# Optimization experiments

Hardware: AMD Instinct MI355X
Metric: run time of the kernel (lower is better)

Reference implementation:

```python
import jax, jax.numpy as jnp
import numpy as np

N_SOC = 100_000   # nodes in social_neighbour_g (== embedding rows)
N_I2U = 50_000    # nodes in item2user_g
E_SOC = 1_600_000
E_I2U = 800_000
F = 128           # embedding_size (num_heads = 1)


def gatv2(src, dst, num_nodes, feat, Ws, bs, Wd, bd, attn):
    """DGL GATv2Conv, num_heads=1, share_weights=False, activation=leaky_relu."""
    el = feat @ Ws + bs                     # [N, F] fc_src
    er = feat @ Wd + bd                     # [N, F] fc_dst
    e = jax.nn.leaky_relu(el[src] + er[dst], 0.2)   # [E, F]
    s = e @ attn                            # [E] attention logits
    # edge softmax grouped by destination node
    m = jax.ops.segment_max(s, dst, num_segments=num_nodes)
    ex = jnp.exp(s - m[dst])
    den = jax.ops.segment_sum(ex, dst, num_segments=num_nodes)
    alpha = ex / den[dst]                   # [E]
    out = jax.ops.segment_sum(el[src] * alpha[:, None], dst, num_segments=num_nodes)
    return jax.nn.leaky_relu(out, 0.01)     # module-level activation (default slope)


def setup_inputs() -> dict:
    key = jax.random.key(0)
    ks = jax.random.split(key, 16)
    sc = 1.0 / np.sqrt(F)
    inp = {
        "embedding": jax.random.normal(ks[0], (N_SOC, F), jnp.float32),
        "i2u_src": jax.random.randint(ks[1], (E_I2U,), 0, N_I2U, jnp.int32),
        "i2u_dst": jax.random.randint(ks[2], (E_I2U,), 0, N_I2U, jnp.int32),
        "i2u_nid": jnp.arange(N_I2U, dtype=jnp.int32),  # unique global IDs of subgraph nodes
        "soc_src": jax.random.randint(ks[3], (E_SOC,), 0, N_SOC, jnp.int32),
        "soc_dst": jax.random.randint(ks[4], (E_SOC,), 0, N_SOC, jnp.int32),
        "Wsrc1": jax.random.normal(ks[5], (F, F), jnp.float32) * sc,
        "bsrc1": jnp.zeros((F,), jnp.float32),
        "Wdst1": jax.random.normal(ks[6], (F, F), jnp.float32) * sc,
        "bdst1": jnp.zeros((F,), jnp.float32),
        "attn1": jax.random.normal(ks[7], (F,), jnp.float32) * sc,
        "Wsrc2": jax.random.normal(ks[8], (F, F), jnp.float32) * sc,
        "bsrc2": jnp.zeros((F,), jnp.float32),
        "Wdst2": jax.random.normal(ks[9], (F, F), jnp.float32) * sc,
        "bdst2": jnp.zeros((F,), jnp.float32),
        "attn2": jax.random.normal(ks[10], (F,), jnp.float32) * sc,
    }
    return inp


def reference(embedding, i2u_src, i2u_dst, i2u_nid, soc_src, soc_dst,
              Wsrc1, bsrc1, Wdst1, bdst1, attn1,
              Wsrc2, bsrc2, Wdst2, bdst2, attn2):
    # social_used_embedding = embedding[item2user_g.ndata['_ID']]
    used = embedding[i2u_nid]                                   # [N_i2u, F]
    h1 = gatv2(i2u_src, i2u_dst, i2u_nid.shape[0], used,
               Wsrc1, bsrc1, Wdst1, bdst1, attn1)               # [N_i2u, F]
    # social_embedding = embedding[social_g.nodes()]  (nodes() == arange(N_soc))
    soc = embedding
    # used_user_id = where(sum(h1, dim=1) != 0); scatter those rows via _ID
    mask = jnp.sum(h1, axis=1) != 0                              # [N_i2u]
    upd = jnp.where(mask[:, None], h1, soc[i2u_nid])
    soc = soc.at[i2u_nid].set(upd)
    out = gatv2(soc_src, soc_dst, soc.shape[0], soc,
                Wsrc2, bsrc2, Wdst2, bdst2, attn2)               # [N_soc, F]
    return out
```

## Files before the change

kernel.cpp:

```cpp
#include <hip/hip_runtime.h>
#include <hip/hip_fp16.h>
#include <math.h>

#define F 128
#define BSHIFT 9
#define BSIZE  512
#define BMAX   200
#define CHUNK  4096
#define PKSTR  12288

#define APAD 8
#define ASTR (F + APAD)

typedef _Float16 half8_t __attribute__((ext_vector_type(8)));
typedef _Float16 half4_t __attribute__((ext_vector_type(4)));
typedef float f32x4 __attribute__((ext_vector_type(4)));

#define PK_ADD(d, a, b) asm("v_pk_add_f16 %0, %1, %2" : "=v"(d) : "v"(a), "v"(b))
#define PK_MUL(d, a, b) asm("v_pk_mul_f16 %0, %1, %2" : "=v"(d) : "v"(a), "v"(b))
#define PK_MAX(d, a, b) asm("v_pk_max_f16 %0, %1, %2" : "=v"(d) : "v"(a), "v"(b))
#define FMA_MIX_LO(acc, h2u, f) \
    asm("v_fma_mix_f32 %0, %1, %2, %0 op_sel_hi:[1,0,0]" : "+v"(acc) : "v"(h2u), "v"(f))
#define FMA_MIX_HI(acc, h2u, f) \
    asm("v_fma_mix_f32 %0, %1, %2, %0 op_sel:[1,0,0] op_sel_hi:[1,0,0]" : "+v"(acc) : "v"(h2u), "v"(f))

__device__ __forceinline__ float row_sum16(float x) {
    int y;
    y = __builtin_amdgcn_update_dpp(0, __float_as_int(x), 0x121, 0xf, 0xf, true);
    x += __int_as_float(y);
    y = __builtin_amdgcn_update_dpp(0, __float_as_int(x), 0x122, 0xf, 0xf, true);
    x += __int_as_float(y);
    y = __builtin_amdgcn_update_dpp(0, __float_as_int(x), 0x124, 0xf, 0xf, true);
    x += __int_as_float(y);
    y = __builtin_amdgcn_update_dpp(0, __float_as_int(x), 0x128, 0xf, 0xf, true);
    x += __int_as_float(y);
    return x;
}

__global__ __launch_bounds__(256) void k_scatter(
        const int* __restrict__ src1, const int* __restrict__ dst1, int E1,
        int* __restrict__ bcur1, unsigned* __restrict__ pk1, int C1,
        const int* __restrict__ src2, const int* __restrict__ dst2, int E2,
        int* __restrict__ bcur2, unsigned* __restrict__ pk2, int C2,
        const int* __restrict__ nid, int Nn, int* __restrict__ inv, int CI,
        const float* __restrict__ Ws1, const float* __restrict__ Wd1,
        const float* __restrict__ bs1, const float* __restrict__ bd1,
        const float* __restrict__ at1,
        __half* __restrict__ wt1, float* __restrict__ bp1, float* __restrict__ ap1,
        const float* __restrict__ Ws2, const float* __restrict__ Wd2,
        const float* __restrict__ bs2, const float* __restrict__ bd2,
        const float* __restrict__ at2,
        __half* __restrict__ wt2, float* __restrict__ bp2, float* __restrict__ ap2) {
    int b = blockIdx.x, t = threadIdx.x;
    __shared__ int hist[BMAX];
    __shared__ int cur[BMAX];
    if (b < C1 + C2) {
        const int* src; const int* dst; int E; int* bcur; unsigned* pk; int c;
        if (b < C1) { src = src1; dst = dst1; E = E1; bcur = bcur1; pk = pk1; c = b; }
        else        { src = src2; dst = dst2; E = E2; bcur = bcur2; pk = pk2; c = b - C1; }
        for (int i = t; i < BMAX; i += 256) hist[i] = 0;
        __syncthreads();
        int e0 = c * CHUNK;
        int dc[CHUNK / 256], sc[CHUNK / 256];
#pragma unroll
        for (int i = 0; i < CHUNK / 256; i++) {
            int e = e0 + t + i * 256;
            if (e < E) {
                int d = dst[e];
                dc[i] = d; sc[i] = src[e];
                atomicAdd(&hist[d >> BSHIFT], 1);
            } else {
                dc[i] = -1;
            }
        }
        __syncthreads();
        for (int i = t; i < BMAX; i += 256) {
            int n = hist[i];
            if (n) cur[i] = atomicAdd(&bcur[i], n);
        }
        __syncthreads();
#pragma unroll
        for (int i = 0; i < CHUNK / 256; i++) {
            int d = dc[i];
            if (d >= 0) {
                int bb = d >> BSHIFT;
                int pos = atomicAdd(&cur[bb], 1);
                if (pos < PKSTR)
                    pk[(size_t)bb * PKSTR + pos] =
                        ((unsigned)(d & (BSIZE - 1)) << 17) | (unsigned)sc[i];
            }
        }
    } else if (b < C1 + C2 + CI) {
        int i0 = (b - C1 - C2) * CHUNK + t;
#pragma unroll
        for (int k = 0; k < CHUNK / 256; k++) {
            int j = i0 + k * 256;
            if (j < Nn) inv[nid[j]] = j;
        }
    } else {
        int wb = b - (C1 + C2 + CI);
        int layer = wb >> 3, bl = wb & 7;
        const float* Ws = layer ? Ws2 : Ws1;
        const float* Wd = layer ? Wd2 : Wd1;
        __half* wt = layer ? wt2 : wt1;
#pragma unroll
        for (int i = 0; i < 16; i++) {
            int e = bl * 4096 + i * 256 + t;
            int n = e >> 7, k = e & 127;
            float v = (n < 128) ? Ws[k * 128 + n] : Wd[k * 128 + (n - 128)];
            wt[(size_t)n * 128 + k] = __float2half(v);
        }
        if (bl == 0) {
            const float* bs = layer ? bs2 : bs1;
            const float* bd = layer ? bd2 : bd1;
            const float* at = layer ? at2 : at1;
            float* bp = layer ? bp2 : bp1;
            float* ap = layer ? ap2 : ap1;
            bp[t] = (t < 128) ? bs[t] : bd[t - 128];
            if (t < 128) ap[t] = at[t] * 1.44269504f;
        }
    }
}

__device__ __forceinline__ void finesort_body(unsigned* __restrict__ pk,
        const int* __restrict__ bcur, int b, int N,
        int* __restrict__ rpb, int* __restrict__ rpe) {
    __shared__ int cnt[BSIZE];
    __shared__ int cur[BSIZE];
    __shared__ int tps[256];
    int t = threadIdx.x;
    int node0 = b << BSHIFT;
    int base = b * PKSTR;
    int ne = bcur[b]; if (ne > PKSTR) ne = PKSTR;
    unsigned* pkb = pk + (size_t)base;
    cnt[t] = 0; cnt[t + 256] = 0;
    __syncthreads();
    unsigned stash[PKSTR / 256];
#pragma unroll
    for (int k = 0; k < PKSTR / 256; k++) {
        int i = t + k * 256;
        unsigned v = 0xFFFFFFFFu;
        if (i < ne) { v = pkb[i]; atomicAdd(&cnt[v >> 17], 1); }
        stash[k] = v;
    }
    __syncthreads();
    int s0 = cnt[2 * t], s1 = cnt[2 * t + 1];
    int tp = s0 + s1;
    tps[t] = tp;
    __syncthreads();
    for (int off = 1; off < 256; off <<= 1) {
        int x = (t >= off) ? tps[t - off] : 0;
        __syncthreads();
        tps[t] += x;
        __syncthreads();
    }
    int excl = tps[t] - tp;
    int c0 = base + excl, c1 = c0 + s0;
    cur[2 * t] = c0; cur[2 * t + 1] = c1;
    int n0 = node0 + 2 * t, n1 = n0 + 1;
    if (n0 < N) { rpb[n0] = c0; rpe[n0] = c0 + s0; }
    if (n1 < N) { rpb[n1] = c1; rpe[n1] = c1 + s1; }
    __syncthreads();
    int* outb = (int*)pk;
#pragma unroll
    for (int k = 0; k < PKSTR / 256; k++) {
        unsigned v = stash[k];
        if (v != 0xFFFFFFFFu) {
            int dl = v >> 17;
            int pos = atomicAdd(&cur[dl], 1);
            outb[pos] = (int)(v & 0x1FFFFu);
        }
    }
}

__device__ __forceinline__ void gemm_mfma_body(int blk,
        const float* __restrict__ emb, const int* __restrict__ nid,
        const float* __restrict__ h1, const int* __restrict__ inv, const int* __restrict__ flag,
        int Nrows,
        const __half* __restrict__ wt, const float* __restrict__ bp,
        __half* __restrict__ el, __half* __restrict__ er) {
    __shared__ _Float16 As[64 * ASTR];
    __shared__ const float* rps[64];
    int t = threadIdx.x;
    int row0 = blk * 64;

    if (t < 64) {
        int grow = row0 + t;
        const float* rowp = nullptr;
        if (grow < Nrows) {
            if (inv) {
                int j = inv[grow];
                rowp = (j >= 0 && flag[j]) ? h1 + (size_t)j * F : emb + (size_t)grow * F;
            } else {
                int asrc = nid ? nid[grow] : grow;
                rowp = emb + (size_t)asrc * F;
            }
        }
        rps[t] = rowp;
    }
    __syncthreads();

#pragma unroll
    for (int i = 0; i < 8; i++) {
        int e = i * 256 + t;
        int r = e >> 5;
        int c = (e & 31) * 4;
        const float* rowp = rps[r];
        float4 v = make_float4(0.f, 0.f, 0.f, 0.f);
        if (rowp) v = *(const float4*)(rowp + c);
        half4_t hv = { (_Float16)v.x, (_Float16)v.y, (_Float16)v.z, (_Float16)v.w };
        *(half4_t*)(As + r * ASTR + c) = hv;
    }
    __syncthreads();

    int lane = t & 63, wave = t >> 6;
    int li = lane & 15, quad = lane >> 4;

    f32x4 acc[4][4];
#pragma unroll
    for (int a = 0; a < 4; a++)
#pragma unroll
        for (int b = 0; b < 4; b++) acc[a][b] = (f32x4){0.f, 0.f, 0.f, 0.f};

    const _Float16* wtp = (const _Float16*)wt;
#pragma unroll
    for (int ks = 0; ks < 4; ks++) {
        half8_t af[4], bf[4];
#pragma unroll
        for (int nt = 0; nt < 4; nt++)
            af[nt] = *(const half8_t*)(As + (nt * 16 + li) * ASTR + ks * 32 + quad * 8);
#pragma unroll
        for (int ft = 0; ft < 4; ft++) {
            int n = wave * 64 + ft * 16 + li;
            bf[ft] = *(const half8_t*)(wtp + (size_t)n * F + ks * 32 + quad * 8);
        }
#pragma unroll
        for (int ft = 0; ft < 4; ft++)
#pragma unroll
            for (int nt = 0; nt < 4; nt++)
                acc[ft][nt] = __builtin_amdgcn_mfma_f32_16x16x32_f16(
                    bf[ft], af[nt], acc[ft][nt], 0, 0, 0);
    }

    __half* dst = (wave < 2) ? el : er;
    int fb = (wave & 1) * 64 + quad * 4;
    f32x4 bv4[4];
#pragma unroll
    for (int ft = 0; ft < 4; ft++)
        bv4[ft] = *(const f32x4*)(bp + wave * 64 + ft * 16 + quad * 4);
#pragma unroll
    for (int nt = 0; nt < 4; nt++) {
        int node = row0 + nt * 16 + li;
        if (node < Nrows) {
#pragma unroll
            for (int ft = 0; ft < 4; ft++) {
                half4_t h4 = { (_Float16)(acc[ft][nt][0] + bv4[ft][0]),
                               (_Float16)(acc[ft][nt][1] + bv4[ft][1]),
                               (_Float16)(acc[ft][nt][2] + bv4[ft][2]),
                               (_Float16)(acc[ft][nt][3] + bv4[ft][3]) };
                *(half4_t*)(dst + (size_t)node * F + fb + ft * 16) = h4;
            }
        }
    }
}

__global__ __launch_bounds__(256, 4) void k_sortg1(
        unsigned* __restrict__ pk1, const int* __restrict__ bcur1, int B1, int N1,
        int* __restrict__ rpb1, int* __restrict__ rpe1,
        unsigned* __restrict__ pk2, const int* __restrict__ bcur2, int B2, int N2,
        int* __restrict__ rpb2, int* __restrict__ rpe2,
        const float* __restrict__ emb, const int* __restrict__ nid, int G1rows,
        const __half* __restrict__ wt1, const float* __restrict__ bp1,
        __half* __restrict__ el1, __half* __restrict__ er1) {
    int blk = blockIdx.x;
    if (blk < B1 + B2) {
        unsigned* pk; const int* bcur; int b, N; int* rpb; int* rpe;
        if (blk < B1) { pk = pk1; bcur = bcur1; b = blk;      N = N1; rpb = rpb1; rpe = rpe1; }
        else          { pk = pk2; bcur = bcur2; b = blk - B1; N = N2; rpb = rpb2; rpe = rpe2; }
        finesort_body(pk, bcur, b, N, rpb, rpe);
    } else {
        gemm_mfma_body(blk - (B1 + B2), emb, nid, nullptr, nullptr, nullptr,
                       G1rows, wt1, bp1, el1, er1);
    }
}

__global__ __launch_bounds__(256, 4) void gemm2_k(
        const float* __restrict__ emb, const float* __restrict__ h1,
        const int* __restrict__ inv, const int* __restrict__ flag, int Nrows,
        const __half* __restrict__ wt, const float* __restrict__ bp,
        __half* __restrict__ el, __half* __restrict__ er) {
    gemm_mfma_body(blockIdx.x, emb, nullptr, h1, inv, flag, Nrows, wt, bp, el, er);
}

__device__ __forceinline__ void agg_core(
        const int* __restrict__ rpb, const int* __restrict__ rpe,
        const int* __restrict__ srcs,
        const __half* __restrict__ el, const __half* __restrict__ er,
        const float* __restrict__ ap, int node, int g, int li,
        float* o, int& beg, int& end) {
    uint4 ru = *(const uint4*)(er + (size_t)node * F + li * 8);
    float av[8];
    *(float4*)(av + 0) = *(const float4*)(ap + li * 8 + 0);
    *(float4*)(av + 4) = *(const float4*)(ap + li * 8 + 4);

    beg = rpb[node]; end = rpe[node];
    float l = 0.f;
    float acc[8];
#pragma unroll
    for (int j = 0; j < 8; j++) acc[j] = 0.f;

    const unsigned C02 = 0x32663266u;

    auto dot_edge = [&](const uint4& V) -> float {
        float p = 0.f;
        unsigned x, y;
        PK_ADD(x, V.x, ru.x); PK_MUL(y, x, C02); PK_MAX(x, x, y);
        FMA_MIX_LO(p, x, av[0]); FMA_MIX_HI(p, x, av[1]);
        PK_ADD(x, V.y, ru.y); PK_MUL(y, x, C02); PK_MAX(x, x, y);
        FMA_MIX_LO(p, x, av[2]); FMA_MIX_HI(p, x, av[3]);
        PK_ADD(x, V.z, ru.z); PK_MUL(y, x, C02); PK_MAX(x, x, y);
        FMA_MIX_LO(p, x, av[4]); FMA_MIX_HI(p, x, av[5]);
        PK_ADD(x, V.w, ru.w); PK_MUL(y, x, C02); PK_MAX(x, x, y);
        FMA_MIX_LO(p, x, av[6]); FMA_MIX_HI(p, x, av[7]);
        return p;
    };
    auto acc_edge = [&](const uint4& V, float ex) {
        FMA_MIX_LO(acc[0], V.x, ex); FMA_MIX_HI(acc[1], V.x, ex);
        FMA_MIX_LO(acc[2], V.y, ex); FMA_MIX_HI(acc[3], V.y, ex);
        FMA_MIX_LO(acc[4], V.z, ex); FMA_MIX_HI(acc[5], V.z, ex);
        FMA_MIX_LO(acc[6], V.w, ex); FMA_MIX_HI(acc[7], V.w, ex);
    };
    auto compute4 = [&](const uint4& A, const uint4& B, const uint4& Cv, const uint4& D,
                        int cb0) {
        int c0 = cb0 + g * 4;
        bool v0 = c0 < end, v1 = c0 + 1 < end, v2 = c0 + 2 < end, v3 = c0 + 3 < end;
        float p0 = dot_edge(A), p1 = dot_edge(B), p2 = dot_edge(Cv), p3 = dot_edge(D);
        p0 = row_sum16(p0); p1 = row_sum16(p1);
        p2 = row_sum16(p2); p3 = row_sum16(p3);
        float x0 = v0 ? __builtin_amdgcn_exp2f(p0) : 0.f;
        float x1 = v1 ? __builtin_amdgcn_exp2f(p1) : 0.f;
        float x2 = v2 ? __builtin_amdgcn_exp2f(p2) : 0.f;
        float x3 = v3 ? __builtin_amdgcn_exp2f(p3) : 0.f;
        l += (x0 + x1) + (x2 + x3);
        acc_edge(A, x0); acc_edge(B, x1); acc_edge(Cv, x2); acc_edge(D, x3);
    };

    const __half* ep = el + li * 8;
    if (beg < end) {
        int e1 = end - 1;
        int I0, I1, I2, I3, J0, J1, J2, J3;
        {
            int a = beg + g * 4;
            I0 = __builtin_nontemporal_load(srcs + (a     < e1 ? a     : e1));
            I1 = __builtin_nontemporal_load(srcs + (a + 1 < e1 ? a + 1 : e1));
            I2 = __builtin_nontemporal_load(srcs + (a + 2 < e1 ? a + 2 : e1));
            I3 = __builtin_nontemporal_load(srcs + (a + 3 < e1 ? a + 3 : e1));
        }
        uint4 R0 = *(const uint4*)(ep + (size_t)I0 * F);
        uint4 R1 = *(const uint4*)(ep + (size_t)I1 * F);
        uint4 R2 = *(const uint4*)(ep + (size_t)I2 * F);
        uint4 R3 = *(const uint4*)(ep + (size_t)I3 * F);
        {
            int a = beg + 8 + g * 4;
            J0 = __builtin_nontemporal_load(srcs + (a     < e1 ? a     : e1));
            J1 = __builtin_nontemporal_load(srcs + (a + 1 < e1 ? a + 1 : e1));
            J2 = __builtin_nontemporal_load(srcs + (a + 2 < e1 ? a + 2 : e1));
            J3 = __builtin_nontemporal_load(srcs + (a + 3 < e1 ? a + 3 : e1));
        }
        int cb = beg;
        for (;;) {
            uint4 S0, S1, S2, S3;
            bool hn = (cb + 8) < end;
            if (hn) {
                S0 = *(const uint4*)(ep + (size_t)J0 * F);
                S1 = *(const uint4*)(ep + (size_t)J1 * F);
                S2 = *(const uint4*)(ep + (size_t)J2 * F);
                S3 = *(const uint4*)(ep + (size_t)J3 * F);
                int a = cb + 16 + g * 4;
                I0 = __builtin_nontemporal_load(srcs + (a     < e1 ? a     : e1));
                I1 = __builtin_nontemporal_load(srcs + (a + 1 < e1 ? a + 1 : e1));
                I2 = __builtin_nontemporal_load(srcs + (a + 2 < e1 ? a + 2 : e1));
                I3 = __builtin_nontemporal_load(srcs + (a + 3 < e1 ? a + 3 : e1));
            }
            compute4(R0, R1, R2, R3, cb);
            cb += 8;
            if (!hn) break;
            bool hn2 = (cb + 8) < end;
            if (hn2) {
                R0 = *(const uint4*)(ep + (size_t)I0 * F);
                R1 = *(const uint4*)(ep + (size_t)I1 * F);
                R2 = *(const uint4*)(ep + (size_t)I2 * F);
                R3 = *(const uint4*)(ep + (size_t)I3 * F);
                int a = cb + 16 + g * 4;
                J0 = __builtin_nontemporal_load(srcs + (a     < e1 ? a     : e1));
                J1 = __builtin_nontemporal_load(srcs + (a + 1 < e1 ? a + 1 : e1));
                J2 = __builtin_nontemporal_load(srcs + (a + 2 < e1 ? a + 2 : e1));
                J3 = __builtin_nontemporal_load(srcs + (a + 3 < e1 ? a + 3 : e1));
            }
            compute4(S0, S1, S2, S3, cb);
            cb += 8;
            if (!hn2) break;
        }
    }

    l += __shfl_xor(l, 16, 64);
#pragma unroll
    for (int j = 0; j < 8; j++) acc[j] += __shfl_xor(acc[j], 16, 64);

    if (end > beg) {
        float inv = 1.f / l;
#pragma unroll
        for (int j = 0; j < 8; j++) {
            float v = acc[j] * inv;
            o[j] = fmaxf(v, 0.01f * v);
        }
    } else {
#pragma unroll
        for (int j = 0; j < 8; j++) o[j] = 0.f;
    }
}

__global__ __launch_bounds__(256) void agg1_k(
        const int* __restrict__ rpb, const int* __restrict__ rpe,
        const int* __restrict__ srcs,
        const __half* __restrict__ el, const __half* __restrict__ er,
        const float* __restrict__ ap, int N,
        float* __restrict__ h1, int* __restrict__ flag) {
    int node = blockIdx.x * 8 + (threadIdx.x >> 5);
    if (node >= N) return;
    int t = threadIdx.x;
    int g = (t >> 4) & 1, li = t & 15;
    float o[8]; int beg, end;
    agg_core(rpb, rpe, srcs, el, er, ap, node, g, li, o, beg, end);

    float tot = 0.f;
#pragma unroll
    for (int j = 0; j < 8; j++) tot += o[j];
    tot = row_sum16(tot);
    if (g == 0) {
        *(float4*)(h1 + (size_t)node * F + li * 8 + 0) = *(float4*)(o + 0);
        *(float4*)(h1 + (size_t)node * F + li * 8 + 4) = *(float4*)(o + 4);
        if (li == 0) flag[node] = (tot != 0.f) ? 1 : 0;
    }
}

__global__ __launch_bounds__(256) void agg2_k(
        const int* __restrict__ rpb, const int* __restrict__ rpe,
        const int* __restrict__ srcs,
        const __half* __restrict__ el, const __half* __restrict__ er,
        const float* __restrict__ ap, int N, float* __restrict__ out) {
    int node = blockIdx.x * 8 + (threadIdx.x >> 5);
    if (node >= N) return;
    int t = threadIdx.x;
    int g = (t >> 4) & 1, li = t & 15;
    float o[8]; int beg, end;
    agg_core(rpb, rpe, srcs, el, er, ap, node, g, li, o, beg, end);
    if (g == 0) {
        *(float4*)(out + (size_t)node * F + li * 8 + 0) = *(float4*)(o + 0);
        *(float4*)(out + (size_t)node * F + li * 8 + 4) = *(float4*)(o + 4);
    }
}

static inline int cdiv(int a, int b) { return (a + b - 1) / b; }

extern "C" void kernel_launch(void* const* d_in, const int* in_sizes, int n_in,
                              void* d_out, int out_size, void* d_ws, size_t ws_size,
                              hipStream_t stream) {
    const float* emb   = (const float*)d_in[0];
    const int* i2u_src = (const int*)d_in[1];
    const int* i2u_dst = (const int*)d_in[2];
    const int* i2u_nid = (const int*)d_in[3];
    const int* soc_src = (const int*)d_in[4];
    const int* soc_dst = (const int*)d_in[5];
    const float* Ws1 = (const float*)d_in[6];
    const float* bs1 = (const float*)d_in[7];
    const float* Wd1 = (const float*)d_in[8];
    const float* bd1 = (const float*)d_in[9];
    const float* at1 = (const float*)d_in[10];
    const float* Ws2 = (const float*)d_in[11];
    const float* bs2 = (const float*)d_in[12];
    const float* Wd2 = (const float*)d_in[13];
    const float* bd2 = (const float*)d_in[14];
    const float* at2 = (const float*)d_in[15];

    const int N_soc = in_sizes[0] / F;
    const int E_i2u = in_sizes[1];
    const int N_i2u = in_sizes[3];
    const int E_soc = in_sizes[4];

    const int B1 = cdiv(N_i2u, BSIZE);
    const int B2 = cdiv(N_soc, BSIZE);
    const int C1 = cdiv(E_i2u, CHUNK);
    const int C2 = cdiv(E_soc, CHUNK);
    const int CI = cdiv(N_i2u, CHUNK);
    const int G1 = cdiv(N_i2u, 64);

    char* p = (char*)d_ws;
    auto carve = [&](size_t bytes) -> char* {
        char* r = p; p += (bytes + 255) & ~(size_t)255; return r;
    };
    __half* el1  = (__half*)carve((size_t)N_i2u * F * 2);
    __half* er1  = (__half*)carve((size_t)N_i2u * F * 2);
    __half* el2  = (__half*)carve((size_t)N_soc * F * 2);
    __half* er2  = (__half*)carve((size_t)N_soc * F * 2);
    float* h1buf = (float*)carve((size_t)N_i2u * F * 4);
    int* flag    = (int*)carve((size_t)N_i2u * 4);
    int* inv     = (int*)carve((size_t)N_soc * 4);

    unsigned* pk1 = (unsigned*)carve((size_t)B1 * PKSTR * 4);
    unsigned* pk2 = (unsigned*)carve((size_t)B2 * PKSTR * 4);
    int* rpb1    = (int*)carve((size_t)N_i2u * 4);
    int* rpe1    = (int*)carve((size_t)N_i2u * 4);
    int* rpb2    = (int*)carve((size_t)N_soc * 4);
    int* rpe2    = (int*)carve((size_t)N_soc * 4);

    int* bcur    = (int*)carve((size_t)(B1 + B2) * 4);
    int* bcur1 = bcur, *bcur2 = bcur + B1;

    __half* wt1  = (__half*)carve((size_t)256 * 128 * 2);
    __half* wt2  = (__half*)carve((size_t)256 * 128 * 2);
    float* bp1   = (float*)carve(256 * 4);
    float* bp2   = (float*)carve(256 * 4);
    float* ap1   = (float*)carve(128 * 4);
    float* ap2   = (float*)carve(128 * 4);

    (void)hipMemsetAsync(bcur, 0, (size_t)(B1 + B2) * 4, stream);
    (void)hipMemsetAsync(inv, 0xFF, (size_t)N_soc * 4, stream);

    k_scatter<<<C1 + C2 + CI + 16, 256, 0, stream>>>(
        i2u_src, i2u_dst, E_i2u, bcur1, pk1, C1,
        soc_src, soc_dst, E_soc, bcur2, pk2, C2,
        i2u_nid, N_i2u, inv, CI,
        Ws1, Wd1, bs1, bd1, at1, wt1, bp1, ap1,
        Ws2, Wd2, bs2, bd2, at2, wt2, bp2, ap2);

    k_sortg1<<<B1 + B2 + G1, 256, 0, stream>>>(
        pk1, bcur1, B1, N_i2u, rpb1, rpe1,
        pk2, bcur2, B2, N_soc, rpb2, rpe2,
        emb, i2u_nid, N_i2u, wt1, bp1, el1, er1);

    agg1_k<<<cdiv(N_i2u, 8), 256, 0, stream>>>(
        rpb1, rpe1, (const int*)pk1, el1, er1, ap1, N_i2u, h1buf, flag);

    gemm2_k<<<cdiv(N_soc, 64), 256, 0, stream>>>(emb, h1buf, inv, flag, N_soc, wt2, bp2, el2, er2);

    agg2_k<<<cdiv(N_soc, 8), 256, 0, stream>>>(
        rpb2, rpe2, (const int*)pk2, el2, er2, ap2, N_soc, (float*)d_out);
}
```

Baseline: 344.9 us.

## Use one 16-lane group per node in aggregation, drop dual-group split

The aggregation kernels change from two 16-lane groups per destination node (each taking alternate 4-edge chunks, then combined by cross-lane shuffles) to a single 16-lane group per node, packing 16 nodes per block. The deep double-buffered prefetch of gathered rows is replaced by a simple loop that only prefetches the next four source indices. The aim is to remove idle half-groups on low-degree nodes and the final shuffle reduction. In exchange each node's edges are processed serially with less memory-level parallelism, since gathered rows are no longer prefetched ahead.

```diff
diff --git a/kernel.cpp b/kernel.cpp
--- a/kernel.cpp
+++ b/kernel.cpp
@@ -296,7 +296,7 @@
         const int* __restrict__ rpb, const int* __restrict__ rpe,
         const int* __restrict__ srcs,
         const __half* __restrict__ el, const __half* __restrict__ er,
-        const float* __restrict__ ap, int node, int g, int li,
+        const float* __restrict__ ap, int node, int li,
         float* o, int& beg, int& end) {
     uint4 ru = *(const uint4*)(er + (size_t)node * F + li * 8);
     float av[8];
@@ -330,82 +330,40 @@
         FMA_MIX_LO(acc[4], V.z, ex); FMA_MIX_HI(acc[5], V.z, ex);
         FMA_MIX_LO(acc[6], V.w, ex); FMA_MIX_HI(acc[7], V.w, ex);
     };
-    auto compute4 = [&](const uint4& A, const uint4& B, const uint4& Cv, const uint4& D,
-                        int cb0) {
-        int c0 = cb0 + g * 4;
-        bool v0 = c0 < end, v1 = c0 + 1 < end, v2 = c0 + 2 < end, v3 = c0 + 3 < end;
-        float p0 = dot_edge(A), p1 = dot_edge(B), p2 = dot_edge(Cv), p3 = dot_edge(D);
-        p0 = row_sum16(p0); p1 = row_sum16(p1);
-        p2 = row_sum16(p2); p3 = row_sum16(p3);
-        float x0 = v0 ? __builtin_amdgcn_exp2f(p0) : 0.f;
-        float x1 = v1 ? __builtin_amdgcn_exp2f(p1) : 0.f;
-        float x2 = v2 ? __builtin_amdgcn_exp2f(p2) : 0.f;
-        float x3 = v3 ? __builtin_amdgcn_exp2f(p3) : 0.f;
-        l += (x0 + x1) + (x2 + x3);
-        acc_edge(A, x0); acc_edge(B, x1); acc_edge(Cv, x2); acc_edge(D, x3);
-    };
 
     const __half* ep = el + li * 8;
     if (beg < end) {
         int e1 = end - 1;
-        int I0, I1, I2, I3, J0, J1, J2, J3;
-        {
-            int a = beg + g * 4;
-            I0 = __builtin_nontemporal_load(srcs + (a     < e1 ? a     : e1));
-            I1 = __builtin_nontemporal_load(srcs + (a + 1 < e1 ? a + 1 : e1));
-            I2 = __builtin_nontemporal_load(srcs + (a + 2 < e1 ? a + 2 : e1));
-            I3 = __builtin_nontemporal_load(srcs + (a + 3 < e1 ? a + 3 : e1));
-        }
-        uint4 R0 = *(const uint4*)(ep + (size_t)I0 * F);
-        uint4 R1 = *(const uint4*)(ep + (size_t)I1 * F);
-        uint4 R2 = *(const uint4*)(ep + (size_t)I2 * F);
-        uint4 R3 = *(const uint4*)(ep + (size_t)I3 * F);
-        {
-            int a = beg + 8 + g * 4;
-            J0 = __builtin_nontemporal_load(srcs + (a     < e1 ? a     : e1));
-            J1 = __builtin_nontemporal_load(srcs + (a + 1 < e1 ? a + 1 : e1));
-            J2 = __builtin_nontemporal_load(srcs + (a + 2 < e1 ? a + 2 : e1));
-            J3 = __builtin_nontemporal_load(srcs + (a + 3 < e1 ? a + 3 : e1));
-        }
-        int cb = beg;
-        for (;;) {
-            uint4 S0, S1, S2, S3;
-            bool hn = (cb + 8) < end;
-            if (hn) {
-                S0 = *(const uint4*)(ep + (size_t)J0 * F);
-                S1 = *(const uint4*)(ep + (size_t)J1 * F);
-                S2 = *(const uint4*)(ep + (size_t)J2 * F);
-                S3 = *(const uint4*)(ep + (size_t)J3 * F);
-                int a = cb + 16 + g * 4;
-                I0 = __builtin_nontemporal_load(srcs + (a     < e1 ? a     : e1));
-                I1 = __builtin_nontemporal_load(srcs + (a + 1 < e1 ? a + 1 : e1));
-                I2 = __builtin_nontemporal_load(srcs + (a + 2 < e1 ? a + 2 : e1));
-                I3 = __builtin_nontemporal_load(srcs + (a + 3 < e1 ? a + 3 : e1));
+        int s0 = __builtin_nontemporal_load(srcs + beg);
+        int s1 = __builtin_nontemporal_load(srcs + (beg + 1 < e1 ? beg + 1 : e1));
+        int s2 = __builtin_nontemporal_load(srcs + (beg + 2 < e1 ? beg + 2 : e1));
+        int s3 = __builtin_nontemporal_load(srcs + (beg + 3 < e1 ? beg + 3 : e1));
+        for (int cb = beg; cb < end; cb += 4) {
+            bool v0 = cb < end, v1 = cb + 1 < end, v2 = cb + 2 < end, v3 = cb + 3 < end;
+            int t0 = s0, t1 = s1, t2 = s2, t3 = s3;
+            int nb = cb + 4;
+            if (nb < end) {
+                s0 = __builtin_nontemporal_load(srcs + (nb     < e1 ? nb     : e1));
+                s1 = __builtin_nontemporal_load(srcs + (nb + 1 < e1 ? nb + 1 : e1));
+                s2 = __builtin_nontemporal_load(srcs + (nb + 2 < e1 ? nb + 2 : e1));
+                s3 = __builtin_nontemporal_load(srcs + (nb + 3 < e1 ? nb + 3 : e1));
             }
-            compute4(R0, R1, R2, R3, cb);
-            cb += 8;
-            if (!hn) break;
-            bool hn2 = (cb + 8) < end;
-            if (hn2) {
-                R0 = *(const uint4*)(ep + (size_t)I0 * F);
-                R1 = *(const uint4*)(ep + (size_t)I1 * F);
-                R2 = *(const uint4*)(ep + (size_t)I2 * F);
-                R3 = *(const uint4*)(ep + (size_t)I3 * F);
-                int a = cb + 16 + g * 4;
-                J0 = __builtin_nontemporal_load(srcs + (a     < e1 ? a     : e1));
-                J1 = __builtin_nontemporal_load(srcs + (a + 1 < e1 ? a + 1 : e1));
-                J2 = __builtin_nontemporal_load(srcs + (a + 2 < e1 ? a + 2 : e1));
-                J3 = __builtin_nontemporal_load(srcs + (a + 3 < e1 ? a + 3 : e1));
-            }
-            compute4(S0, S1, S2, S3, cb);
-            cb += 8;
-            if (!hn2) break;
-        }
-    }
-
-    l += __shfl_xor(l, 16, 64);
-#pragma unroll
-    for (int j = 0; j < 8; j++) acc[j] += __shfl_xor(acc[j], 16, 64);
+            uint4 A  = *(const uint4*)(ep + (size_t)t0 * F);
+            uint4 B  = *(const uint4*)(ep + (size_t)t1 * F);
+            uint4 Cv = *(const uint4*)(ep + (size_t)t2 * F);
+            uint4 D  = *(const uint4*)(ep + (size_t)t3 * F);
+
+            float p0 = dot_edge(A), p1 = dot_edge(B), p2 = dot_edge(Cv), p3 = dot_edge(D);
+            p0 = row_sum16(p0); p1 = row_sum16(p1);
+            p2 = row_sum16(p2); p3 = row_sum16(p3);
+            float x0 = v0 ? __builtin_amdgcn_exp2f(p0) : 0.f;
+            float x1 = v1 ? __builtin_amdgcn_exp2f(p1) : 0.f;
+            float x2 = v2 ? __builtin_amdgcn_exp2f(p2) : 0.f;
+            float x3 = v3 ? __builtin_amdgcn_exp2f(p3) : 0.f;
+            l += (x0 + x1) + (x2 + x3);
+            acc_edge(A, x0); acc_edge(B, x1); acc_edge(Cv, x2); acc_edge(D, x3);
+        }
+    }
 
     if (end > beg) {
         float inv = 1.f / l;
@@ -426,22 +384,19 @@
         const __half* __restrict__ el, const __half* __restrict__ er,
         const float* __restrict__ ap, int N,
         float* __restrict__ h1, int* __restrict__ flag) {
-    int node = blockIdx.x * 8 + (threadIdx.x >> 5);
+    int node = blockIdx.x * 16 + (threadIdx.x >> 4);
     if (node >= N) return;
-    int t = threadIdx.x;
-    int g = (t >> 4) & 1, li = t & 15;
+    int li = threadIdx.x & 15;
     float o[8]; int beg, end;
-    agg_core(rpb, rpe, srcs, el, er, ap, node, g, li, o, beg, end);
+    agg_core(rpb, rpe, srcs, el, er, ap, node, li, o, beg, end);
 
     float tot = 0.f;
 #pragma unroll
     for (int j = 0; j < 8; j++) tot += o[j];
     tot = row_sum16(tot);
-    if (g == 0) {
-        *(float4*)(h1 + (size_t)node * F + li * 8 + 0) = *(float4*)(o + 0);
-        *(float4*)(h1 + (size_t)node * F + li * 8 + 4) = *(float4*)(o + 4);
-        if (li == 0) flag[node] = (tot != 0.f) ? 1 : 0;
-    }
+    *(float4*)(h1 + (size_t)node * F + li * 8 + 0) = *(float4*)(o + 0);
+    *(float4*)(h1 + (size_t)node * F + li * 8 + 4) = *(float4*)(o + 4);
+    if (li == 0) flag[node] = (tot != 0.f) ? 1 : 0;
 }
 
 __global__ __launch_bounds__(256) void agg2_k(
@@ -449,16 +404,13 @@
         const int* __restrict__ srcs,
         const __half* __restrict__ el, const __half* __restrict__ er,
         const float* __restrict__ ap, int N, float* __restrict__ out) {
-    int node = blockIdx.x * 8 + (threadIdx.x >> 5);
+    int node = blockIdx.x * 16 + (threadIdx.x >> 4);
     if (node >= N) return;
-    int t = threadIdx.x;
-    int g = (t >> 4) & 1, li = t & 15;
+    int li = threadIdx.x & 15;
     float o[8]; int beg, end;
-    agg_core(rpb, rpe, srcs, el, er, ap, node, g, li, o, beg, end);
-    if (g == 0) {
-        *(float4*)(out + (size_t)node * F + li * 8 + 0) = *(float4*)(o + 0);
-        *(float4*)(out + (size_t)node * F + li * 8 + 4) = *(float4*)(o + 4);
-    }
+    agg_core(rpb, rpe, srcs, el, er, ap, node, li, o, beg, end);
+    *(float4*)(out + (size_t)node * F + li * 8 + 0) = *(float4*)(o + 0);
+    *(float4*)(out + (size_t)node * F + li * 8 + 4) = *(float4*)(o + 4);
 }
 
 static inline int cdiv(int a, int b) { return (a + b - 1) / b; }
@@ -539,11 +491,11 @@
         pk2, bcur2, B2, N_soc, rpb2, rpe2,
         emb, i2u_nid, N_i2u, wt1, bp1, el1, er1);
 
-    agg1_k<<<cdiv(N_i2u, 8), 256, 0, stream>>>(
+    agg1_k<<<cdiv(N_i2u, 16), 256, 0, stream>>>(
         rpb1, rpe1, (const int*)pk1, el1, er1, ap1, N_i2u, h1buf, flag);
 
     gemm2_k<<<cdiv(N_soc, 64), 256, 0, stream>>>(emb, h1buf, inv, flag, N_soc, wt2, bp2, el2, er2);
 
-    agg2_k<<<cdiv(N_soc, 8), 256, 0, stream>>>(
+    agg2_k<<<cdiv(N_soc, 16), 256, 0, stream>>>(
         rpb2, rpe2, (const int*)pk2, el2, er2, ap2, N_soc, (float*)d_out);
 }
```

Result: slower. 356.5 us (+3.4%).
